# Kernel optimization log

Measured on AMD Instinct MI355X. Metric: run time of the kernel, lower is better.

The kernel has to match this reference:

```python
import jax, jax.numpy as jnp
import numpy as np

B, T, D = 2, 2048, 2048
H, HD, RD = 16, 192, 64
CD = HD - RD          # 128 content dims per head
QR, DL = 768, 512     # q lora rank, kv latent dim
THETA = 10000.0


def setup_inputs() -> dict:
    key = jax.random.key(0)
    ks = jax.random.split(key, 9)
    s = 0.02
    return {
        "x": jax.random.normal(ks[0], (B, T, D), jnp.float32),
        "wq_down": jax.random.normal(ks[1], (D, QR), jnp.float32) * s,
        "wq_up": jax.random.normal(ks[2], (QR, H * CD), jnp.float32) * s,
        "wq_rope": jax.random.normal(ks[3], (D, H * RD), jnp.float32) * s,
        "wkv_down": jax.random.normal(ks[4], (D, DL), jnp.float32) * s,
        "wk_up": jax.random.normal(ks[5], (DL, H * CD), jnp.float32) * s,
        "wv_up": jax.random.normal(ks[6], (DL, H * HD), jnp.float32) * s,
        "wk_rope": jax.random.normal(ks[7], (D, H * RD), jnp.float32) * s,
        "wo": jax.random.normal(ks[8], (H * HD, D), jnp.float32) * s,
    }


def _rope_tables(seq_len):
    inv = 1.0 / (THETA ** (jnp.arange(0, RD, 2, dtype=jnp.float32) / RD))  # [RD/2]
    ang = jnp.arange(seq_len, dtype=jnp.float32)[:, None] * inv[None, :]  # [T, RD/2]
    return jnp.cos(ang), jnp.sin(ang)


def _apply_rope(x, cos, sin):
    # x: [B,H,T,RD]; cos/sin: [T,RD/2] broadcast over B,H
    d = RD // 2
    x1, x2 = x[..., :d], x[..., d:]
    return jnp.concatenate([x1 * cos - x2 * sin, x1 * sin + x2 * cos], axis=-1)


def reference(x, wq_down, wq_up, wq_rope, wkv_down, wk_up, wv_up, wk_rope, wo):
    # projections
    q_c = (x @ wq_down) @ wq_up                       # [B,T,H*CD]
    q_p = x @ wq_rope                                 # [B,T,H*RD]
    latent = x @ wkv_down                             # [B,T,DL]
    k_c = latent @ wk_up                              # [B,T,H*CD]
    k_p = x @ wk_rope                                 # [B,T,H*RD]
    v = latent @ wv_up                                # [B,T,H*HD]

    def heads(t, d):
        return t.reshape(B, T, H, d).transpose(0, 2, 1, 3)  # [B,H,T,d]

    q_c, q_p = heads(q_c, CD), heads(q_p, RD)
    k_c, k_p = heads(k_c, CD), heads(k_p, RD)
    v = heads(v, HD)

    cos, sin = _rope_tables(T)
    q_p = _apply_rope(q_p, cos, sin)
    k_p = _apply_rope(k_p, cos, sin)

    q = jnp.concatenate([q_c, q_p], axis=-1)          # [B,H,T,HD]
    k = jnp.concatenate([k_c, k_p], axis=-1)          # [B,H,T,HD]

    scale = 1.0 / jnp.sqrt(jnp.asarray(HD, q.dtype))
    scores = jnp.einsum("bhqd,bhkd->bhqk", q, k) * scale
    causal = jnp.tril(jnp.ones((T, T), dtype=bool))
    scores = jnp.where(causal, scores, jnp.finfo(scores.dtype).min)
    attn = jax.nn.softmax(scores, axis=-1)
    out = jnp.einsum("bhqk,bhkd->bhqd", attn, v)      # [B,H,T,HD]
    out = out.transpose(0, 2, 1, 3).reshape(B, T, H * HD)
    return out @ wo                                   # [B,T,D]
```

## Files before the change

kernel.cpp:

```cpp
#include <hip/hip_runtime.h>
#include <hip/hip_bf16.h>
#include <cstdint>
#include <cstddef>

typedef __bf16 bf16_t;
typedef __bf16 bf16x8 __attribute__((ext_vector_type(8)));
typedef float f32x4 __attribute__((ext_vector_type(4)));

#define MFMA16(a, b, c) __builtin_amdgcn_mfma_f32_16x16x32_bf16((a), (b), (c), 0, 0, 0)

__device__ __forceinline__ void gload_lds16(const void* g, void* l) {
  __builtin_amdgcn_global_load_lds((__attribute__((address_space(1))) void*)(g),
                                   (__attribute__((address_space(3))) void*)(l),
                                   16, 0, 0);
}

__device__ __forceinline__ uint32_t pkbf(float lo, float hi) {
  union { bf16_t h[2]; uint32_t u; } u2;
  u2.h[0] = (bf16_t)lo; u2.h[1] = (bf16_t)hi;
  return u2.u;
}

__global__ __launch_bounds__(256) void cvt_f32_to_bf16(const float* __restrict__ in,
                                                       bf16_t* __restrict__ out) {
  size_t i = ((size_t)blockIdx.x * 256 + threadIdx.x) * 4;
  float4 v = *(const float4*)(in + i);
  bf16_t o0 = (bf16_t)v.x, o1 = (bf16_t)v.y, o2 = (bf16_t)v.z, o3 = (bf16_t)v.w;
  bf16_t o[4] = {o0, o1, o2, o3};
  *(uint2*)(out + i) = *(uint2*)o;
}

__global__ __launch_bounds__(256) void transpose_w(const float* __restrict__ in,
                                                   bf16_t* __restrict__ out, int R, int C) {
  __shared__ bf16_t tile[32][33];
  int c0 = blockIdx.x * 32, r0 = blockIdx.y * 32;
  int tx = threadIdx.x, ty = threadIdx.y;
#pragma unroll
  for (int s = 0; s < 4; s++) {
    int r = ty + s * 8;
    tile[r][tx] = (bf16_t)in[(size_t)(r0 + r) * C + c0 + tx];
  }
  __syncthreads();
#pragma unroll
  for (int s = 0; s < 4; s++) {
    int r = ty + s * 8;
    out[(size_t)(c0 + r) * R + r0 + tx] = tile[tx][r];
  }
}

__global__ __launch_bounds__(256) void transpose_v_kernel(const bf16_t* __restrict__ v,
                                                          bf16_t* __restrict__ vt) {
  __shared__ bf16_t tile[32][33];
  int bh = blockIdx.z;
  int t0 = blockIdx.x * 32, d0 = blockIdx.y * 32;
  int tx = threadIdx.x, ty = threadIdx.y;
  const bf16_t* src = v + (size_t)(bh >> 4) * 2048 * 3072 + (bh & 15) * 192;
#pragma unroll
  for (int s = 0; s < 4; s++) {
    int t = ty + s * 8;
    tile[t][tx] = src[(size_t)(t0 + t) * 3072 + d0 + tx];
  }
  __syncthreads();
  bf16_t* dst = vt + (size_t)bh * 192 * 2048;
#pragma unroll
  for (int s = 0; s < 4; s++) {
    int d = ty + s * 8;
    dst[(size_t)(d0 + d) * 2048 + t0 + tx] = tile[tx][d];
  }
}

__global__ __launch_bounds__(256) void rope_inplace(bf16_t* __restrict__ buf) {
  int idx = blockIdx.x * 256 + threadIdx.x;
  int j = idx & 31;
  int h = (idx >> 5) & 15;
  int row = idx >> 9;
  int t = row & 2047;
  size_t base = (size_t)row * 3072 + h * 192 + 128;
  float inv = expf(-(float)j * 0.28782313662425574f);
  float ang = (float)t * inv;
  float c, s;
  sincosf(ang, &s, &c);
  float x1 = (float)buf[base + j];
  float x2 = (float)buf[base + j + 32];
  buf[base + j]      = (bf16_t)(x1 * c - x2 * s);
  buf[base + j + 32] = (bf16_t)(x1 * s + x2 * c);
}

template <int MODE>
__global__ __launch_bounds__(256) void gemm_bt(const bf16_t* __restrict__ A, int lda,
                                               const bf16_t* __restrict__ Bt,
                                               void* __restrict__ C0, void* __restrict__ C1,
                                               void* __restrict__ C2, int K, int ldc) {
  __shared__ __align__(16) bf16_t sA[128 * 64];
  __shared__ __align__(16) bf16_t sB[128 * 64];
  const int tid = threadIdx.x;
  const int l = tid & 63, w = tid >> 6;
  const int l15 = l & 15, l4 = l >> 4;
  const int wr = w >> 1, wc = w & 1;
  const int m0 = blockIdx.y * 128, n0 = blockIdx.x * 128;

  f32x4 acc[4][4] = {};

  for (int kt = 0; kt < K; kt += 64) {
#pragma unroll
    for (int r = 0; r < 4; r++) {
      int i = r * 256 + tid;
      int row = i >> 3, cl = i & 7;
      int cg = cl ^ (row & 7);
      const bf16_t* srcA = A + (size_t)(m0 + row) * lda + kt + cg * 8;
      const bf16_t* srcB = Bt + (size_t)(n0 + row) * K + kt + cg * 8;
      char* dstA = (char*)sA + (size_t)(r * 256 + w * 64) * 16;
      char* dstB = (char*)sB + (size_t)(r * 256 + w * 64) * 16;
      gload_lds16(srcA, dstA);
      gload_lds16(srcB, dstB);
    }
    __syncthreads();
#pragma unroll
    for (int ks = 0; ks < 2; ks++) {
      bf16x8 af[4], bfr[4];
#pragma unroll
      for (int mf = 0; mf < 4; mf++) {
        int row = wr * 64 + mf * 16 + l15;
        int cl = (ks * 4 + l4) ^ (row & 7);
        af[mf] = *(const bf16x8*)(sA + row * 64 + cl * 8);
      }
#pragma unroll
      for (int nf = 0; nf < 4; nf++) {
        int row = wc * 64 + nf * 16 + l15;
        int cl = (ks * 4 + l4) ^ (row & 7);
        bfr[nf] = *(const bf16x8*)(sB + row * 64 + cl * 8);
      }
#pragma unroll
      for (int mf = 0; mf < 4; mf++)
#pragma unroll
        for (int nf = 0; nf < 4; nf++)
          acc[mf][nf] = MFMA16(af[mf], bfr[nf], acc[mf][nf]);
    }
    __syncthreads();
  }

#pragma unroll
  for (int mf = 0; mf < 4; mf++)
#pragma unroll
    for (int nf = 0; nf < 4; nf++)
#pragma unroll
      for (int r = 0; r < 4; r++) {
        int m = m0 + wr * 64 + mf * 16 + l4 * 4 + r;
        int n = n0 + wc * 64 + nf * 16 + l15;
        float v = acc[mf][nf][r];
        if constexpr (MODE == 1) {
          ((float*)C0)[(size_t)m * ldc + n] = v;
        } else if constexpr (MODE == 2) {
          ((bf16_t*)C0)[(size_t)m * 3072 + (n >> 7) * 192 + (n & 127)] = (bf16_t)v;
        } else if constexpr (MODE == 4) {
          if (n < 1280) {
            ((bf16_t*)C0)[(size_t)m * 1280 + n] = (bf16_t)v;
          } else if (n < 2304) {
            int nn = n - 1280;
            ((bf16_t*)C1)[(size_t)m * 3072 + (nn >> 6) * 192 + 128 + (nn & 63)] = (bf16_t)v;
          } else {
            int nn = n - 2304;
            ((bf16_t*)C2)[(size_t)m * 3072 + (nn >> 6) * 192 + 128 + (nn & 63)] = (bf16_t)v;
          }
        } else {
          if (n < 2048) {
            ((bf16_t*)C0)[(size_t)m * 3072 + (n >> 7) * 192 + (n & 127)] = (bf16_t)v;
          } else {
            ((bf16_t*)C1)[(size_t)m * 3072 + (n - 2048)] = (bf16_t)v;
          }
        }
      }
}

__global__ __launch_bounds__(512, 2) void attn_kernel(const bf16_t* __restrict__ q,
                                                      const bf16_t* __restrict__ kbuf,
                                                      const bf16_t* __restrict__ vt,
                                                      bf16_t* __restrict__ ao) {
  __shared__ __align__(16) bf16_t sK[2][64][192];
  __shared__ __align__(16) bf16_t sV[2][192][64];

  const int tid = threadIdx.x, l = tid & 63, w = tid >> 6;
  const int l15 = l & 15, l4 = (l >> 4) & 3;
  const int bh = blockIdx.x & 31;
  const int c = blockIdx.x >> 5;
  const int b = bh >> 4, h = bh & 15;
  const int ca = c, cb = 15 - c;
  const int ra = ca * 128 + w * 16;
  const int rb = cb * 128 + w * 16;
  const int tga = 2 * ca + (w >> 2);
  const int tgb = 2 * cb + (w >> 2);

  const bf16_t* qp = q + (size_t)b * 2048 * 3072 + h * 192;
  const bf16_t* kp = kbuf + (size_t)b * 2048 * 3072 + h * 192;
  const bf16_t* vp = vt + (size_t)bh * 192 * 2048;

  bf16x8 qf[2][6];
#pragma unroll
  for (int kd = 0; kd < 6; kd++) {
    qf[0][kd] = *(const bf16x8*)(qp + (size_t)(ra + l15) * 3072 + kd * 32 + l4 * 8);
    qf[1][kd] = *(const bf16x8*)(qp + (size_t)(rb + l15) * 3072 + kd * 32 + l4 * 8);
  }

  f32x4 o[2][12] = {};
  float mrow[2] = {-__builtin_inff(), -__builtin_inff()};
  float lrow[2] = {0.0f, 0.0f};

  const float scale = 0.07216878364870322f;
  const float THR = 7.0f;
  const int nkt = 2 * cb + 2;
  const int src0 = l15 + ((l4 & 1) << 5);
  const int src1 = src0 + 16;
  const bool hibank = (l4 & 2) != 0;

#define STAGE(BB, KT)                                                               \
  {                                                                                 \
    const int k0s = (KT) * 64;                                                      \
    _Pragma("unroll")                                                               \
    for (int r = 0; r < 3; r++) {                                                   \
      int i = r * 512 + tid;                                                        \
      int row = i / 24, cc = i % 24;                                                \
      int g = cc - (row & 7) * 3;                                                   \
      if (g < 0) g += 24;                                                           \
      gload_lds16(kp + (size_t)(k0s + row) * 3072 + g * 8,                          \
                  (char*)&sK[BB][0][0] + (size_t)(r * 512 + w * 64) * 16);          \
    }                                                                               \
    _Pragma("unroll")                                                               \
    for (int r = 0; r < 3; r++) {                                                   \
      int i = r * 512 + tid;                                                        \
      int d = i >> 3, cc = i & 7;                                                   \
      gload_lds16(vp + (size_t)d * 2048 + k0s + (cc ^ (d & 7)) * 8,                 \
                  (char*)&sV[BB][0][0] + (size_t)(r * 512 + w * 64) * 16);          \
    }                                                                               \
  }

  STAGE(0, 0)
  __syncthreads();

  for (int kt = 0; kt < nkt; kt++) {
    const int bb = kt & 1;
    const int k0 = kt * 64;
    const bool act_a = (kt <= tga);
    const bool act_b = (kt <= tgb);
    if (kt + 1 < nkt) STAGE(bb ^ 1, kt + 1)

    f32x4 s[2][4] = {};
#pragma unroll
    for (int kd = 0; kd < 6; kd++) {
      bf16x8 bk[4];
#pragma unroll
      for (int nf = 0; nf < 4; nf++) {
        int row = nf * 16 + l15;
        int cl = kd * 4 + l4 + (row & 7) * 3;
        if (cl >= 24) cl -= 24;
        bk[nf] = *(const bf16x8*)(&sK[bb][row][cl * 8]);
      }
      if (act_b) {
#pragma unroll
        for (int nf = 0; nf < 4; nf++)
          s[1][nf] = MFMA16(bk[nf], qf[1][kd], s[1][nf]);
      }
      if (act_a) {
#pragma unroll
        for (int nf = 0; nf < 4; nf++)
          s[0][nf] = MFMA16(bk[nf], qf[0][kd], s[0][nf]);
      }
    }

    bf16x8 pa[2][2] = {};

#define SOFTMAX_CHUNK(c, rbase, tg)                                                    \
    {                                                                                  \
      const bool diag = (kt == (tg));                                                  \
      _Pragma("unroll")                                                                \
      for (int nf = 0; nf < 4; nf++)                                                   \
        _Pragma("unroll")                                                              \
        for (int r = 0; r < 4; r++) {                                                  \
          float sv = s[c][nf][r] * scale;                                              \
          if (diag) {                                                                  \
            int ktok = k0 + nf * 16 + l4 * 4 + r;                                      \
            if (ktok > (rbase) + l15) sv = -__builtin_inff();                          \
          }                                                                            \
          s[c][nf][r] = sv;                                                            \
        }                                                                              \
      float m_in = s[c][0][0];                                                         \
      _Pragma("unroll")                                                                \
      for (int nf = 0; nf < 4; nf++)                                                   \
        _Pragma("unroll")                                                              \
        for (int r = 0; r < 4; r++)                                                    \
          if (nf | r) m_in = fmaxf(m_in, s[c][nf][r]);                                 \
      m_in = fmaxf(m_in, __shfl_xor(m_in, 16));                                        \
      m_in = fmaxf(m_in, __shfl_xor(m_in, 32));                                        \
      if (!__all(m_in - mrow[c] <= THR)) {                                             \
        float mn = fmaxf(mrow[c], m_in);                                               \
        float alpha = __expf(mrow[c] - mn);                                            \
        mrow[c] = mn;                                                                  \
        lrow[c] *= alpha;                                                              \
        f32x4 av;                                                                      \
        _Pragma("unroll")                                                              \
        for (int r = 0; r < 4; r++) av[r] = __shfl(alpha, l4 * 4 + r);                 \
        _Pragma("unroll")                                                              \
        for (int nf2 = 0; nf2 < 12; nf2++) o[c][nf2] *= av;                            \
      }                                                                                \
      float rs = 0.0f;                                                                 \
      _Pragma("unroll")                                                                \
      for (int nf = 0; nf < 4; nf++)                                                   \
        _Pragma("unroll")                                                              \
        for (int r = 0; r < 4; r++) {                                                  \
          float pv = __expf(s[c][nf][r] - mrow[c]);                                    \
          s[c][nf][r] = pv;                                                            \
          rs += pv;                                                                    \
        }                                                                              \
      rs += __shfl_xor(rs, 16);                                                        \
      rs += __shfl_xor(rs, 32);                                                        \
      lrow[c] += rs;                                                                   \
      uint32_t wq[8];                                                                  \
      _Pragma("unroll")                                                                \
      for (int nf = 0; nf < 4; nf++) {                                                 \
        wq[nf * 2 + 0] = pkbf(s[c][nf][0], s[c][nf][1]);                               \
        wq[nf * 2 + 1] = pkbf(s[c][nf][2], s[c][nf][3]);                               \
      }                                                                                \
      _Pragma("unroll")                                                                \
      for (int ks = 0; ks < 2; ks++) {                                                 \
        uint32_t A0 = __shfl(wq[(2 * ks) * 2 + 0], src0);                              \
        uint32_t A1 = __shfl(wq[(2 * ks) * 2 + 1], src0);                              \
        uint32_t B0 = __shfl(wq[(2 * ks + 1) * 2 + 0], src0);                          \
        uint32_t B1 = __shfl(wq[(2 * ks + 1) * 2 + 1], src0);                          \
        uint32_t C0w = __shfl(wq[(2 * ks) * 2 + 0], src1);                             \
        uint32_t C1w = __shfl(wq[(2 * ks) * 2 + 1], src1);                             \
        uint32_t D0 = __shfl(wq[(2 * ks + 1) * 2 + 0], src1);                          \
        uint32_t D1 = __shfl(wq[(2 * ks + 1) * 2 + 1], src1);                          \
        union { uint32_t u[4]; bf16x8 v; } fr;                                         \
        fr.u[0] = hibank ? B0 : A0;                                                    \
        fr.u[1] = hibank ? B1 : A1;                                                    \
        fr.u[2] = hibank ? D0 : C0w;                                                   \
        fr.u[3] = hibank ? D1 : C1w;                                                   \
        pa[c][ks] = fr.v;                                                              \
      }                                                                                \
    }

    if (act_b) SOFTMAX_CHUNK(1, rb, tgb)
    if (act_a) SOFTMAX_CHUNK(0, ra, tga)
#undef SOFTMAX_CHUNK

#pragma unroll
    for (int ks = 0; ks < 2; ks++) {
#pragma unroll
      for (int nf2 = 0; nf2 < 12; nf2++) {
        int d = nf2 * 16 + l15;
        int cl = (ks * 4 + l4) ^ (d & 7);
        bf16x8 vb = *(const bf16x8*)(&sV[bb][d][cl * 8]);
        if (act_b) o[1][nf2] = MFMA16(pa[1][ks], vb, o[1][nf2]);
        if (act_a) o[0][nf2] = MFMA16(pa[0][ks], vb, o[0][nf2]);
      }
    }

    __syncthreads();
  }
#undef STAGE

#pragma unroll
  for (int mf = 0; mf < 2; mf++) {
    const int rbase = (mf == 0) ? ra : rb;
#pragma unroll
    for (int r = 0; r < 4; r++) {
      float lv = __shfl(lrow[mf], l4 * 4 + r);
      float inv = 1.0f / lv;
      int qrow = rbase + l4 * 4 + r;
#pragma unroll
      for (int nf2 = 0; nf2 < 12; nf2++) {
        int d = nf2 * 16 + l15;
        ao[(size_t)(b * 2048 + qrow) * 3072 + h * 192 + d] = (bf16_t)(o[mf][nf2][r] * inv);
      }
    }
  }
}

extern "C" void kernel_launch(void* const* d_in, const int* in_sizes, int n_in,
                              void* d_out, int out_size, void* d_ws, size_t ws_size,
                              hipStream_t stream) {
  const float* x       = (const float*)d_in[0];
  const float* wq_down = (const float*)d_in[1];
  const float* wq_up   = (const float*)d_in[2];
  const float* wq_rope = (const float*)d_in[3];
  const float* wkv_down= (const float*)d_in[4];
  const float* wk_up   = (const float*)d_in[5];
  const float* wv_up   = (const float*)d_in[6];
  const float* wk_rope = (const float*)d_in[7];
  const float* wo      = (const float*)d_in[8];
  float* out = (float*)d_out;

  char* p = (char*)d_ws;
  auto take = [&](size_t elems) { bf16_t* r = (bf16_t*)p; p += elems * 2; return r; };
  bf16_t* xb    = take(4096ull * 2048);
  bf16_t* fw1   = take(3328ull * 2048);
  bf16_t* wqu_t = take(2048ull * 768);
  bf16_t* fw2   = take(5120ull * 512);
  bf16_t* wo_t  = take(2048ull * 3072);
  bf16_t* qkvd  = take(4096ull * 1280);
  bf16_t* qbuf  = take(4096ull * 3072);
  bf16_t* kbuf  = take(4096ull * 3072);
  bf16_t* vbuf  = take(4096ull * 3072);
  bf16_t* vt    = take(4096ull * 3072);
  bf16_t* ao    = vbuf;

  dim3 tb(32, 8);
  cvt_f32_to_bf16<<<8192, 256, 0, stream>>>(x, xb);
  transpose_w<<<dim3(24, 64), tb, 0, stream>>>(wq_down,  fw1,                 2048, 768);
  transpose_w<<<dim3(16, 64), tb, 0, stream>>>(wkv_down, fw1 + 768ull * 2048, 2048, 512);
  transpose_w<<<dim3(32, 64), tb, 0, stream>>>(wq_rope,  fw1 + 1280ull * 2048,2048, 1024);
  transpose_w<<<dim3(32, 64), tb, 0, stream>>>(wk_rope,  fw1 + 2304ull * 2048,2048, 1024);
  transpose_w<<<dim3(64, 24), tb, 0, stream>>>(wq_up,    wqu_t,               768, 2048);
  transpose_w<<<dim3(64, 16), tb, 0, stream>>>(wk_up,    fw2,                 512, 2048);
  transpose_w<<<dim3(96, 16), tb, 0, stream>>>(wv_up,    fw2 + 2048ull * 512, 512, 3072);
  transpose_w<<<dim3(64, 96), tb, 0, stream>>>(wo,       wo_t,                3072, 2048);

  gemm_bt<4><<<dim3(26, 32), 256, 0, stream>>>(xb, 2048, fw1, qkvd, qbuf, kbuf, 2048, 0);
  gemm_bt<2><<<dim3(16, 32), 256, 0, stream>>>(qkvd, 1280, wqu_t, qbuf, nullptr, nullptr, 768, 0);
  gemm_bt<5><<<dim3(40, 32), 256, 0, stream>>>(qkvd + 768, 1280, fw2, kbuf, vbuf, nullptr, 512, 0);

  rope_inplace<<<8192, 256, 0, stream>>>(qbuf);
  rope_inplace<<<8192, 256, 0, stream>>>(kbuf);
  transpose_v_kernel<<<dim3(64, 6, 32), tb, 0, stream>>>(vbuf, vt);

  attn_kernel<<<256, 512, 0, stream>>>(qbuf, kbuf, vt, ao);

  gemm_bt<1><<<dim3(16, 32), 256, 0, stream>>>(ao, 3072, wo_t, out, nullptr, nullptr, 3072, 2048);
}
```

Baseline: 386.8 us.

## Split attention blocks into 256-thread single-tile blocks with single-buffered K

Replaces the 512-thread attention block, which paired a low and a high query tile for load balancing, with 512 blocks of 256 threads. Each block handles one 128-row query tile as two 64-row halves per wave. K staging becomes single-buffered to halve its LDS footprint, so the next K/V prefetch is issued only after the QK^T MFMAs behind an extra barrier. This is meant to raise occupancy and cut LDS per block, at the cost of less overlap between prefetch and QK^T and reliance on the scheduler to balance the causal workload.

After: 422.9 us. 9.3% more time.

```diff
diff --git a/kernel.cpp b/kernel.cpp
--- a/kernel.cpp
+++ b/kernel.cpp
@@ -25,8 +25,7 @@
                                                        bf16_t* __restrict__ out) {
   size_t i = ((size_t)blockIdx.x * 256 + threadIdx.x) * 4;
   float4 v = *(const float4*)(in + i);
-  bf16_t o0 = (bf16_t)v.x, o1 = (bf16_t)v.y, o2 = (bf16_t)v.z, o3 = (bf16_t)v.w;
-  bf16_t o[4] = {o0, o1, o2, o3};
+  bf16_t o[4] = {(bf16_t)v.x, (bf16_t)v.y, (bf16_t)v.z, (bf16_t)v.w};
   *(uint2*)(out + i) = *(uint2*)o;
 }
 
@@ -172,23 +171,24 @@
       }
 }
 
-__global__ __launch_bounds__(512, 2) void attn_kernel(const bf16_t* __restrict__ q,
+__global__ __launch_bounds__(256, 2) void attn_kernel(const bf16_t* __restrict__ q,
                                                       const bf16_t* __restrict__ kbuf,
                                                       const bf16_t* __restrict__ vt,
                                                       bf16_t* __restrict__ ao) {
-  __shared__ __align__(16) bf16_t sK[2][64][192];
+  __shared__ __align__(16) bf16_t sK[64][192];
   __shared__ __align__(16) bf16_t sV[2][192][64];
 
   const int tid = threadIdx.x, l = tid & 63, w = tid >> 6;
   const int l15 = l & 15, l4 = (l >> 4) & 3;
-  const int bh = blockIdx.x & 31;
-  const int c = blockIdx.x >> 5;
+  const int bid = blockIdx.x;
+  const int half = bid >> 8, rr = bid & 255;
+  const int bh = rr & 31;
+  const int qi = half ? (15 - (rr >> 5)) : (rr >> 5);
   const int b = bh >> 4, h = bh & 15;
-  const int ca = c, cb = 15 - c;
-  const int ra = ca * 128 + w * 16;
-  const int rb = cb * 128 + w * 16;
-  const int tga = 2 * ca + (w >> 2);
-  const int tgb = 2 * cb + (w >> 2);
+  const int rA = qi * 128 + w * 16;
+  const int rB = rA + 64;
+  const int tgA = 2 * qi;
+  const int nkt = 2 * qi + 2;
 
   const bf16_t* qp = q + (size_t)b * 2048 * 3072 + h * 192;
   const bf16_t* kp = kbuf + (size_t)b * 2048 * 3072 + h * 192;
@@ -197,8 +197,8 @@
   bf16x8 qf[2][6];
 #pragma unroll
   for (int kd = 0; kd < 6; kd++) {
-    qf[0][kd] = *(const bf16x8*)(qp + (size_t)(ra + l15) * 3072 + kd * 32 + l4 * 8);
-    qf[1][kd] = *(const bf16x8*)(qp + (size_t)(rb + l15) * 3072 + kd * 32 + l4 * 8);
+    qf[0][kd] = *(const bf16x8*)(qp + (size_t)(rA + l15) * 3072 + kd * 32 + l4 * 8);
+    qf[1][kd] = *(const bf16x8*)(qp + (size_t)(rB + l15) * 3072 + kd * 32 + l4 * 8);
   }
 
   f32x4 o[2][12] = {};
@@ -207,41 +207,43 @@
 
   const float scale = 0.07216878364870322f;
   const float THR = 7.0f;
-  const int nkt = 2 * cb + 2;
   const int src0 = l15 + ((l4 & 1) << 5);
   const int src1 = src0 + 16;
   const bool hibank = (l4 & 2) != 0;
 
-#define STAGE(BB, KT)                                                               \
+#define STAGE_K(KT)                                                                 \
   {                                                                                 \
     const int k0s = (KT) * 64;                                                      \
     _Pragma("unroll")                                                               \
-    for (int r = 0; r < 3; r++) {                                                   \
-      int i = r * 512 + tid;                                                        \
+    for (int r = 0; r < 6; r++) {                                                   \
+      int i = r * 256 + tid;                                                        \
       int row = i / 24, cc = i % 24;                                                \
       int g = cc - (row & 7) * 3;                                                   \
       if (g < 0) g += 24;                                                           \
       gload_lds16(kp + (size_t)(k0s + row) * 3072 + g * 8,                          \
-                  (char*)&sK[BB][0][0] + (size_t)(r * 512 + w * 64) * 16);          \
+                  (char*)&sK[0][0] + (size_t)(r * 256 + w * 64) * 16);              \
     }                                                                               \
+  }
+#define STAGE_V(KT, VB)                                                             \
+  {                                                                                 \
+    const int k0s = (KT) * 64;                                                      \
     _Pragma("unroll")                                                               \
-    for (int r = 0; r < 3; r++) {                                                   \
-      int i = r * 512 + tid;                                                        \
+    for (int r = 0; r < 6; r++) {                                                   \
+      int i = r * 256 + tid;                                                        \
       int d = i >> 3, cc = i & 7;                                                   \
       gload_lds16(vp + (size_t)d * 2048 + k0s + (cc ^ (d & 7)) * 8,                 \
-                  (char*)&sV[BB][0][0] + (size_t)(r * 512 + w * 64) * 16);          \
+                  (char*)&sV[VB][0][0] + (size_t)(r * 256 + w * 64) * 16);          \
     }                                                                               \
   }
 
-  STAGE(0, 0)
+  STAGE_K(0)
+  STAGE_V(0, 0)
   __syncthreads();
 
   for (int kt = 0; kt < nkt; kt++) {
     const int bb = kt & 1;
     const int k0 = kt * 64;
-    const bool act_a = (kt <= tga);
-    const bool act_b = (kt <= tgb);
-    if (kt + 1 < nkt) STAGE(bb ^ 1, kt + 1)
+    const bool act_a = (kt <= tgA);
 
     f32x4 s[2][4] = {};
 #pragma unroll
@@ -252,18 +254,22 @@
         int row = nf * 16 + l15;
         int cl = kd * 4 + l4 + (row & 7) * 3;
         if (cl >= 24) cl -= 24;
-        bk[nf] = *(const bf16x8*)(&sK[bb][row][cl * 8]);
-      }
-      if (act_b) {
-#pragma unroll
-        for (int nf = 0; nf < 4; nf++)
-          s[1][nf] = MFMA16(bk[nf], qf[1][kd], s[1][nf]);
-      }
+        bk[nf] = *(const bf16x8*)(&sK[row][cl * 8]);
+      }
+#pragma unroll
+      for (int nf = 0; nf < 4; nf++)
+        s[1][nf] = MFMA16(bk[nf], qf[1][kd], s[1][nf]);
       if (act_a) {
 #pragma unroll
         for (int nf = 0; nf < 4; nf++)
           s[0][nf] = MFMA16(bk[nf], qf[0][kd], s[0][nf]);
       }
+    }
+
+    __syncthreads();
+    if (kt + 1 < nkt) {
+      STAGE_K(kt + 1)
+      STAGE_V(kt + 1, bb ^ 1)
     }
 
     bf16x8 pa[2][2] = {};
@@ -338,8 +344,8 @@
       }                                                                                \
     }
 
-    if (act_b) SOFTMAX_CHUNK(1, rb, tgb)
-    if (act_a) SOFTMAX_CHUNK(0, ra, tga)
+    SOFTMAX_CHUNK(1, rB, nkt - 1)
+    if (act_a) SOFTMAX_CHUNK(0, rA, tgA)
 #undef SOFTMAX_CHUNK
 
 #pragma unroll
@@ -349,18 +355,19 @@
         int d = nf2 * 16 + l15;
         int cl = (ks * 4 + l4) ^ (d & 7);
         bf16x8 vb = *(const bf16x8*)(&sV[bb][d][cl * 8]);
-        if (act_b) o[1][nf2] = MFMA16(pa[1][ks], vb, o[1][nf2]);
+        o[1][nf2] = MFMA16(pa[1][ks], vb, o[1][nf2]);
         if (act_a) o[0][nf2] = MFMA16(pa[0][ks], vb, o[0][nf2]);
       }
     }
 
     __syncthreads();
   }
-#undef STAGE
+#undef STAGE_K
+#undef STAGE_V
 
 #pragma unroll
   for (int mf = 0; mf < 2; mf++) {
-    const int rbase = (mf == 0) ? ra : rb;
+    const int rbase = (mf == 0) ? rA : rB;
 #pragma unroll
     for (int r = 0; r < 4; r++) {
       float lv = __shfl(lrow[mf], l4 * 4 + r);
@@ -422,7 +429,7 @@
   rope_inplace<<<8192, 256, 0, stream>>>(kbuf);
   transpose_v_kernel<<<dim3(64, 6, 32), tb, 0, stream>>>(vbuf, vt);
 
-  attn_kernel<<<256, 512, 0, stream>>>(qbuf, kbuf, vt, ao);
+  attn_kernel<<<512, 256, 0, stream>>>(qbuf, kbuf, vt, ao);
 
   gemm_bt<1><<<dim3(16, 32), 256, 0, stream>>>(ao, 3072, wo_t, out, nullptr, nullptr, 3072, 2048);
 }
```
